# Kernel tuning notes

Hardware: AMD Instinct MI355X
Metric: run time of the kernel (lower is better)

The kernel has to match this reference:

```python
import jax, jax.numpy as jnp
import numpy as np
from math import sqrt

N_USERS = 60000
N_ITEMS = 40000
D = 64
B = 3
LAYERS = 2
E = 600000
BATCH = 2048
N_NODES = (N_USERS + 1) + (N_ITEMS + 1)
REG_WEIGHT = 1e-3
BPR_GAMMA = 1e-10


def setup_inputs() -> dict:
    key = jax.random.key(0)
    k0, k1, k2, k3, k4 = jax.random.split(key, 5)
    user_emb = jax.random.normal(k0, (N_USERS + 1, D), jnp.float32) * 0.1
    item_emb = jax.random.normal(k1, (N_ITEMS + 1, D), jnp.float32) * 0.1
    W = jnp.ones((B,), jnp.float32)
    edge_users = jax.random.randint(k2, (B, E), 1, N_USERS + 1)
    edge_items = jax.random.randint(k3, (B, E), 1, N_ITEMS + 1)
    batch_data = jax.random.randint(k4, (BATCH, B, 3), 1, N_ITEMS + 1)
    return dict(user_emb=user_emb, item_emb=item_emb, W=W,
                edge_users=edge_users, edge_items=edge_items,
                batch_data=batch_data)


def _lightgcn(emb, eu, ei, layers):
    # bipartite undirected graph: users <-> items (items offset by N_USERS+1)
    it = ei + (N_USERS + 1)
    src = jnp.concatenate([eu, it])
    dst = jnp.concatenate([it, eu])
    deg = jax.ops.segment_sum(jnp.ones_like(src, jnp.float32), src, N_NODES)
    norm = jax.lax.rsqrt(jnp.maximum(deg[src], 1.0)) * jax.lax.rsqrt(jnp.maximum(deg[dst], 1.0))
    out = emb
    cur = emb
    for _ in range(layers):
        cur = jax.ops.segment_sum(cur[src] * norm[:, None], dst, N_NODES)
        out = out + cur
    return out / (layers + 1)


def _mutual_attention(f):
    # f: [N, B, D]
    S = jnp.einsum('nid,njd->nij', f, f)          # [N, B, B] pairwise scores
    last = S[:, B - 1:B, :]                        # [N, 1, B]
    proj = S[:, :B - 1, :]                         # [N, B-1, B]
    # (last * proj) * last / (last^2 + eps)   (dim-1 is size 1, sums/norms trivial)
    clear = (last * proj) * last / (last * last + 1e-12)   # [N, B-1, B]
    scores = jnp.sum(clear, axis=1, keepdims=True) + last   # [N, 1, B]
    all_scores = jnp.concatenate([clear, scores], axis=1)   # [N, B, B]
    att = jax.nn.softmax(all_scores / sqrt(D), axis=-1)
    return jnp.einsum('nij,njd->nid', att, f)


def reference(user_emb, item_emb, W, edge_users, edge_items, batch_data):
    total0 = jnp.concatenate([user_emb, item_emb], axis=0)   # [N_NODES, D]
    # global graph = union of all behaviors
    g_eu = edge_users.reshape(-1)
    g_ei = edge_items.reshape(-1)
    all_emb = _lightgcn(total0, g_eu, g_ei, LAYERS)
    # per-behavior propagation
    u_list, i_list = [], []
    for b in range(B):
        eb = _lightgcn(all_emb, edge_users[b], edge_items[b], LAYERS)
        u_list.append(eb[:N_USERS + 1])
        i_list.append(eb[N_USERS + 1:])
    all_user = jnp.stack(u_list, axis=1)   # [n_users+1, B, D]
    all_item = jnp.stack(i_list, axis=1)   # [n_items+1, B, D]
    all_user = _mutual_attention(all_user)
    # item behaviour degree: interactions per item per behavior
    ones = jnp.ones((E,), jnp.float32)
    ibd = jnp.stack([jax.ops.segment_sum(ones, edge_items[b], N_ITEMS + 1)
                     for b in range(B)], axis=1)   # [n_items+1, B]
    weight = ibd * W
    weight = weight / (jnp.sum(weight, axis=1, keepdims=True) + 1e-8)
    item_final = jnp.sum(all_item * weight[:, :, None], axis=1)   # [n_items+1, D]
    total_loss = jnp.float32(0.0)
    for b in range(B):
        users = batch_data[:, b, 0]
        items = batch_data[:, b, 1:3]
        uf = all_user[:, b][users][:, None, :]      # [batch, 1, D]
        itf = item_final[items]                      # [batch, 2, D]
        scores = jnp.sum(uf * itf, axis=2)           # [batch, 2]
        total_loss = total_loss - jnp.mean(
            jnp.log(BPR_GAMMA + jax.nn.sigmoid(scores[:, 0] - scores[:, 1])))
    emb_loss = (jnp.linalg.norm(user_emb) + jnp.linalg.norm(item_emb)) / (N_ITEMS + 1)
    return total_loss + REG_WEIGHT * emb_loss
```

## Files before the change

### kernel.cpp

```cpp
#include <hip/hip_runtime.h>
#include <hip/hip_bf16.h>
#include <math.h>

#define NUQ 60001
#define NIQ 40001
#define NNQ 100002
#define DQ  64
#define EQ  600000
#define BQ  3
#define BATCHQ 2048
#define ROWW 32
#define NSLOT (BATCHQ * BQ)
#define NPAD 100004
#define ADJB 1200000
#define BLK_ELE 2048
#define NBLK ((NNQ + BLK_ELE - 1) / BLK_ELE)
#define RANGE 392
#define NRANGE 256
#define NBINS (BQ * NRANGE)
#define NBLKA 256
#define EPB ((BQ * EQ + NBLKA - 1) / NBLKA)

typedef float f32x2 __attribute__((ext_vector_type(2)));

__device__ __forceinline__ float wave_sum(float v) {
#pragma unroll
  for (int m = 32; m >= 1; m >>= 1) v += __shfl_xor(v, m, 64);
  return v;
}
__device__ __forceinline__ int wave_sum_i(int v) {
#pragma unroll
  for (int m = 32; m >= 1; m >>= 1) v += __shfl_xor(v, m, 64);
  return v;
}

__device__ __forceinline__ unsigned pack_bf2(float lo, float hi) {
  unsigned a = __float_as_uint(lo);
  unsigned b = __float_as_uint(hi);
  a = (a + 0x7FFFu + ((a >> 16) & 1u)) >> 16;
  b = (b + 0x7FFFu + ((b >> 16) & 1u)) >> 16;
  return a | (b << 16);
}
__device__ __forceinline__ float unpk_lo(unsigned u) { return __uint_as_float(u << 16); }
__device__ __forceinline__ float unpk_hi(unsigned u) { return __uint_as_float(u & 0xFFFF0000u); }

__device__ __forceinline__ void ntst_u32(unsigned* p, unsigned v) { __builtin_nontemporal_store(v, p); }
__device__ __forceinline__ void ntst_f32(float* p, float v) { __builtin_nontemporal_store(v, p); }
__device__ __forceinline__ float ntld_f32(const float* p) { return __builtin_nontemporal_load(p); }

__global__ void zero_i_k(int* __restrict__ p, int n) {
  int tid = blockIdx.x * blockDim.x + threadIdx.x;
  int stride = gridDim.x * blockDim.x;
  for (int i = tid; i < n; i += stride) p[i] = 0;
}

__global__ void sumsq_k(const float* __restrict__ p, int n, float* __restrict__ acc) {
  int tid = blockIdx.x * blockDim.x + threadIdx.x;
  int stride = gridDim.x * blockDim.x;
  float s = 0.f;
  for (int i = tid; i < n; i += stride) { float v = p[i]; s += v * v; }
  s = wave_sum(s);
  __shared__ float ws[4];
  if ((threadIdx.x & 63) == 0) ws[threadIdx.x >> 6] = s;
  __syncthreads();
  if (threadIdx.x == 0) atomicAdd(acc, ws[0] + ws[1] + ws[2] + ws[3]);
}

__global__ void binc_k(const int* __restrict__ eu, const int* __restrict__ ei,
                       unsigned* __restrict__ counts) {
  __shared__ unsigned h[NBINS];
  for (int i = threadIdx.x; i < NBINS; i += 256) h[i] = 0u;
  __syncthreads();
  int base = blockIdx.x * EPB;
  int end = base + EPB;
  if (end > BQ * EQ) end = BQ * EQ;
  for (int idx = base + threadIdx.x; idx < end; idx += 256) {
    int b = idx / EQ;
    int u = eu[idx];
    int it = ei[idx] + NUQ;
    atomicAdd(&h[b * NRANGE + u / RANGE], 1u);
    atomicAdd(&h[b * NRANGE + it / RANGE], 1u);
  }
  __syncthreads();
  for (int i = threadIdx.x; i < NBINS; i += 256)
    counts[(size_t)blockIdx.x * NBINS + i] = h[i];
}

__global__ void binscan1_k(const unsigned* __restrict__ counts,
                           unsigned* __restrict__ offs, unsigned* __restrict__ bintot) {
  int bin = blockIdx.x;
  int t = threadIdx.x;
  int lane = t & 63, wid = t >> 6;
  unsigned v = counts[(size_t)t * NBINS + bin];
  unsigned incl = v;
#pragma unroll
  for (int off = 1; off < 64; off <<= 1) {
    unsigned x = __shfl_up(incl, off, 64);
    if (lane >= off) incl += x;
  }
  __shared__ unsigned wsum[4];
  if (lane == 63) wsum[wid] = incl;
  __syncthreads();
  if (t == 0) {
    unsigned s = 0;
#pragma unroll
    for (int w = 0; w < 4; ++w) { unsigned x = wsum[w]; wsum[w] = s; s += x; }
  }
  __syncthreads();
  unsigned excl = incl - v + wsum[wid];
  offs[(size_t)t * NBINS + bin] = excl;
  if (t == 255) bintot[bin] = excl + v;
}

__global__ void binscan2_k(const unsigned* __restrict__ bintot,
                           unsigned* __restrict__ binstart) {
  int t = threadIdx.x;
  int lane = t & 63, wid = t >> 6;
  unsigned c0 = bintot[t * 3 + 0], c1 = bintot[t * 3 + 1], c2 = bintot[t * 3 + 2];
  unsigned tsum = c0 + c1 + c2;
  unsigned incl = tsum;
#pragma unroll
  for (int off = 1; off < 64; off <<= 1) {
    unsigned x = __shfl_up(incl, off, 64);
    if (lane >= off) incl += x;
  }
  __shared__ unsigned wsum[4];
  if (lane == 63) wsum[wid] = incl;
  __syncthreads();
  if (t == 0) {
    unsigned s = 0;
#pragma unroll
    for (int w = 0; w < 4; ++w) { unsigned x = wsum[w]; wsum[w] = s; s += x; }
  }
  __syncthreads();
  unsigned run = incl - tsum + wsum[wid];
  binstart[t * 3 + 0] = run; run += c0;
  binstart[t * 3 + 1] = run; run += c1;
  binstart[t * 3 + 2] = run; run += c2;
  if (t == 255) binstart[NBINS] = run;
}

__global__ void binfill_k(const int* __restrict__ eu, const int* __restrict__ ei,
                          const unsigned* __restrict__ offs,
                          const unsigned* __restrict__ binstart,
                          unsigned* __restrict__ records) {
  __shared__ unsigned cur[NBINS];
  for (int i = threadIdx.x; i < NBINS; i += 256)
    cur[i] = binstart[i] + offs[(size_t)blockIdx.x * NBINS + i];
  __syncthreads();
  int base = blockIdx.x * EPB;
  int end = base + EPB;
  if (end > BQ * EQ) end = BQ * EQ;
  for (int idx = base + threadIdx.x; idx < end; idx += 256) {
    int b = idx / EQ;
    int u = eu[idx];
    int itl = ei[idx];
    int it = itl + NUQ;
    unsigned p = atomicAdd(&cur[b * NRANGE + u / RANGE], 1u);
    records[p] = ((unsigned)(u % RANGE) << 16) | (unsigned)itl;
    unsigned q = atomicAdd(&cur[b * NRANGE + it / RANGE], 1u);
    records[q] = ((unsigned)(it % RANGE) << 16) | (unsigned)u;
  }
}

__global__ void bindeg_k(const unsigned* __restrict__ records,
                         const unsigned* __restrict__ binstart,
                         int* __restrict__ degB) {
  int bin = blockIdx.x;
  int b = bin / NRANGE;
  int r0 = (bin % NRANGE) * RANGE;
  __shared__ int h[RANGE];
  for (int i = threadIdx.x; i < RANGE; i += 256) h[i] = 0;
  __syncthreads();
  unsigned rs = binstart[bin], re = binstart[bin + 1];
  for (unsigned j = rs + threadIdx.x; j < re; j += 256)
    atomicAdd(&h[records[j] >> 16], 1);
  __syncthreads();
  int nval = NNQ - r0;
  if (nval > RANGE) nval = RANGE;
  int* deg = degB + (size_t)b * NPAD;
  for (int i = threadIdx.x; i < nval; i += 256) deg[r0 + i] = h[i];
}

__global__ void scan_p1_k(const int* __restrict__ degB, int* __restrict__ partial) {
  int b = blockIdx.x / NBLK;
  int blk = blockIdx.x % NBLK;
  const int* deg = degB + (size_t)b * NPAD;
  int base = blk * BLK_ELE + threadIdx.x * 8;
  int s = 0;
#pragma unroll
  for (int i = 0; i < 8; ++i) { int idx = base + i; if (idx < NNQ) s += deg[idx]; }
  s = wave_sum_i(s);
  __shared__ int lds[4];
  int wid = threadIdx.x >> 6;
  if ((threadIdx.x & 63) == 0) lds[wid] = s;
  __syncthreads();
  if (threadIdx.x == 0) partial[b * NBLK + blk] = lds[0] + lds[1] + lds[2] + lds[3];
}

__global__ void scan_p2_k(int* __restrict__ partial, int* __restrict__ rowptrB) {
  int wid = threadIdx.x >> 6;
  int lane = threadIdx.x & 63;
  if (wid >= BQ) return;
  int v = (lane < NBLK) ? partial[wid * NBLK + lane] : 0;
  int orig = v;
#pragma unroll
  for (int off = 1; off < 64; off <<= 1) {
    int t = __shfl_up(v, off, 64);
    if (lane >= off) v += t;
  }
  if (lane < NBLK) partial[wid * NBLK + lane] = v - orig;
  if (lane == NBLK - 1) rowptrB[(size_t)wid * NPAD + NNQ] = v;
}

__global__ void scan_p3_k(const int* __restrict__ degB, const int* __restrict__ partial,
                          int* __restrict__ rowptrB, float* __restrict__ invsqB) {
  int b = blockIdx.x / NBLK;
  int blk = blockIdx.x % NBLK;
  const int* deg = degB + (size_t)b * NPAD;
  int* rowptr = rowptrB + (size_t)b * NPAD;
  float* invsq = invsqB + (size_t)b * NPAD;
  int base = blk * BLK_ELE + threadIdx.x * 8;
  int d[8];
  int tsum = 0;
#pragma unroll
  for (int i = 0; i < 8; ++i) {
    int idx = base + i;
    d[i] = (idx < NNQ) ? deg[idx] : 0;
    tsum += d[i];
  }
  int lane = threadIdx.x & 63;
  int wid = threadIdx.x >> 6;
  int incl = tsum;
#pragma unroll
  for (int off = 1; off < 64; off <<= 1) {
    int t = __shfl_up(incl, off, 64);
    if (lane >= off) incl += t;
  }
  int excl = incl - tsum;
  __shared__ int lds[4];
  if (lane == 63) lds[wid] = incl;
  __syncthreads();
  if (threadIdx.x == 0) {
    int s = 0;
#pragma unroll
    for (int w = 0; w < 4; ++w) { int t = lds[w]; lds[w] = s; s += t; }
  }
  __syncthreads();
  int run = excl + lds[wid] + partial[b * NBLK + blk];
#pragma unroll
  for (int i = 0; i < 8; ++i) {
    int idx = base + i;
    if (idx < NNQ) {
      rowptr[idx] = run;
      run += d[i];
      invsq[idx] = rsqrtf(fmaxf((float)d[i], 1.f));
    }
  }
}

__global__ void invsqg_k(const int* __restrict__ degB, float* __restrict__ invsqG) {
  int n = blockIdx.x * blockDim.x + threadIdx.x;
  if (n >= NNQ) return;
  int dg = degB[n] + degB[NPAD + n] + degB[2 * NPAD + n];
  invsqG[n] = rsqrtf(fmaxf((float)dg, 1.f));
}

__global__ void binscat_k(const unsigned* __restrict__ records,
                          const unsigned* __restrict__ binstart,
                          const int* __restrict__ rowptrB,
                          unsigned short* __restrict__ adjB) {
  int bin = blockIdx.x;
  int b = bin / NRANGE;
  int r0 = (bin % NRANGE) * RANGE;
  int nval = NNQ - r0;
  if (nval > RANGE) nval = RANGE;
  __shared__ int cur[RANGE];
  const int* rowptr = rowptrB + (size_t)b * NPAD;
  for (int i = threadIdx.x; i < nval; i += 256) cur[i] = rowptr[r0 + i];
  __syncthreads();
  unsigned rs = binstart[bin], re = binstart[bin + 1];
  unsigned short* adj = adjB + (size_t)b * ADJB;
  for (unsigned j = rs + threadIdx.x; j < re; j += 256) {
    unsigned rec = records[j];
    int dl = rec >> 16;
    int pos = atomicAdd(&cur[dl], 1);
    adj[pos] = (unsigned short)(rec & 0xFFFFu);
  }
}

__global__ void pack_emb_k(const float* __restrict__ ue, const float* __restrict__ ie,
                           unsigned* __restrict__ E0) {
  int idx = blockIdx.x * blockDim.x + threadIdx.x;
  if (idx >= NNQ * ROWW) return;
  int n = idx >> 5, k = idx & 31;
  const float* src = (n < NUQ) ? (ue + (size_t)n * DQ) : (ie + (size_t)(n - NUQ) * DQ);
  float a = src[2 * k], b = src[2 * k + 1];
  ntst_u32(&E0[idx], pack_bf2(a, b));
}


__device__ __forceinline__ void gather_w32(const unsigned* __restrict__ S,
                                           const unsigned short* __restrict__ adj,
                                           const float* __restrict__ invsq,
                                           int start, int end, int offs,
                                           int l5, int g32, unsigned k4,
                                           float& alo, float& ahi) {
  for (int j0 = start; j0 < end; j0 += 32) {
    int nloc = end - j0;
    if (nloc > 32) nloc = 32;
    unsigned boff = (unsigned)offs << 7;
    float w = 0.f;
    if (l5 < nloc) {
      int a = (int)adj[j0 + l5] + offs;
      boff = (unsigned)a << 7;
      w = invsq[a];
    }
    for (int j = 0; j < nloc; j += 8) {
#pragma unroll
      for (int m = 0; m < 8; ++m) {
        int jj = j + m + g32;
        unsigned bo = (unsigned)__shfl((int)boff, jj, 64) + k4;
        float ww = __shfl(w, jj, 64);
        unsigned dd = *(const unsigned*)((const char*)S + bo);
        alo += ww * unpk_lo(dd);
        ahi += ww * unpk_hi(dd);
      }
    }
  }
}

__device__ __forceinline__ void gather3w32(const unsigned* __restrict__ S,
                                           const unsigned short* __restrict__ adjB,
                                           const float* __restrict__ wtab,
                                           int s0, int d0, int s1, int d1,
                                           int s2, int d2, int offs,
                                           int l5, int g32, unsigned k4,
                                           float& alo, float& ahi) {
  int D = d0 + d1 + d2;
  int d01 = d0 + d1;
  for (int j0 = 0; j0 < D; j0 += 32) {
    int nloc = D - j0;
    if (nloc > 32) nloc = 32;
    unsigned boff = (unsigned)offs << 7;
    float w = 0.f;
    int l = j0 + l5;
    if (l < D) {
      int idx;
      if (l < d0)       idx = s0 + l;
      else if (l < d01) idx = ADJB + s1 + (l - d0);
      else              idx = 2 * ADJB + s2 + (l - d01);
      int a = (int)adjB[idx] + offs;
      boff = (unsigned)a << 7;
      w = wtab[a];
    }
    for (int j = 0; j < nloc; j += 8) {
#pragma unroll
      for (int m = 0; m < 8; ++m) {
        int jj = j + m + g32;
        unsigned bo = (unsigned)__shfl((int)boff, jj, 64) + k4;
        float ww = __shfl(w, jj, 64);
        unsigned dd = *(const unsigned*)((const char*)S + bo);
        alo += ww * unpk_lo(dd);
        ahi += ww * unpk_hi(dd);
      }
    }
  }
}

__global__ void g_l1_k(const unsigned* __restrict__ E0, unsigned* __restrict__ T1,
                       const int* __restrict__ rowptrB, const unsigned short* __restrict__ adjB,
                       const float* __restrict__ invsqG) {
  int wv = (blockIdx.x * blockDim.x + threadIdx.x) >> 6;
  int lane = threadIdx.x & 63;
  int g = lane >> 5;
  int node = wv * 2 + g;
  if (node >= NNQ) return;
  int l5 = lane & 31, g32 = g << 5;
  unsigned k4 = (unsigned)l5 << 2;
  int offs = (node < NUQ) ? NUQ : 0;
  int s0 = rowptrB[node], d0 = rowptrB[node + 1] - s0;
  int s1 = rowptrB[NPAD + node], d1 = rowptrB[NPAD + node + 1] - s1;
  int s2 = rowptrB[2 * NPAD + node], d2 = rowptrB[2 * NPAD + node + 1] - s2;
  float alo = 0.f, ahi = 0.f;
  gather3w32(E0, adjB, invsqG, s0, d0, s1, d1, s2, d2, offs, l5, g32, k4, alo, ahi);
  float s = invsqG[node];
  ntst_u32(&T1[(size_t)node * ROWW + l5], pack_bf2(alo * s, ahi * s));
}

__global__ void g_l2c_k(const unsigned* __restrict__ E0, const unsigned* __restrict__ T1,
                        unsigned* __restrict__ C,
                        const int* __restrict__ rowptrB, const unsigned short* __restrict__ adjB,
                        const float* __restrict__ invsqG) {
  int wv = (blockIdx.x * blockDim.x + threadIdx.x) >> 6;
  int lane = threadIdx.x & 63;
  int g = lane >> 5;
  int node = wv * 2 + g;
  if (node >= NNQ) return;
  int l5 = lane & 31, g32 = g << 5;
  unsigned k4 = (unsigned)l5 << 2;
  int offs = (node < NUQ) ? NUQ : 0;
  int s0 = rowptrB[node], d0 = rowptrB[node + 1] - s0;
  int s1 = rowptrB[NPAD + node], d1 = rowptrB[NPAD + node + 1] - s1;
  int s2 = rowptrB[2 * NPAD + node], d2 = rowptrB[2 * NPAD + node + 1] - s2;
  float alo = 0.f, ahi = 0.f;
  gather3w32(T1, adjB, invsqG, s0, d0, s1, d1, s2, d2, offs, l5, g32, k4, alo, ahi);
  float s = invsqG[node];
  size_t rb = (size_t)node * ROWW + l5;
  unsigned e0 = E0[rb];
  unsigned t1 = T1[rb];
  float clo = (unpk_lo(e0) + unpk_lo(t1) + alo * s) * (1.f / 3.f);
  float chi = (unpk_hi(e0) + unpk_hi(t1) + ahi * s) * (1.f / 3.f);
  ntst_u32(&C[rb], pack_bf2(clo, chi));
}

__global__ void b_l1_k(const unsigned* __restrict__ C, unsigned* __restrict__ T1B,
                       const int* __restrict__ rowptrB, const unsigned short* __restrict__ adjB,
                       const float* __restrict__ invsqB) {
  int wv = (blockIdx.x * blockDim.x + threadIdx.x) >> 6;
  int lane = threadIdx.x & 63;
  int g = lane >> 5;
  int node = wv * 2 + g;
  if (node >= NNQ) return;
  int b = blockIdx.y;
  const int* rowptr = rowptrB + (size_t)b * NPAD;
  const float* iv = invsqB + (size_t)b * NPAD;
  int l5 = lane & 31, g32 = g << 5;
  unsigned k4 = (unsigned)l5 << 2;
  int offs = (node < NUQ) ? NUQ : 0;
  float alo = 0.f, ahi = 0.f;
  gather_w32(C, adjB + (size_t)b * ADJB, iv, rowptr[node], rowptr[node + 1], offs, l5, g32, k4, alo, ahi);
  float s = iv[node];
  ntst_u32(&T1B[(size_t)b * NNQ * ROWW + (size_t)node * ROWW + l5], pack_bf2(alo * s, ahi * s));
}

__global__ void slot_users_k(const unsigned* __restrict__ C, const unsigned* __restrict__ T1B,
                             const int* __restrict__ rowptrB, const unsigned short* __restrict__ adjB,
                             const float* __restrict__ invsqB,
                             const int* __restrict__ batch, float* __restrict__ UG) {
  int wv = (blockIdx.x * blockDim.x + threadIdx.x) >> 6;
  int lane = threadIdx.x & 63;
  int g = lane >> 5;
  int slot = wv * 2 + g;
  if (slot >= NSLOT) return;
  int b = blockIdx.y;
  const int* rp = rowptrB + (size_t)b * NPAD;
  const float* iv = invsqB + (size_t)b * NPAD;
  const unsigned* T1 = T1B + (size_t)b * NNQ * ROWW;
  int u = batch[slot * 3 + 0];
  int l5 = lane & 31, g32 = g << 5;
  unsigned k4 = (unsigned)l5 << 2;
  float alo = 0.f, ahi = 0.f;
  gather_w32(T1, adjB + (size_t)b * ADJB, iv, rp[u], rp[u + 1], NUQ, l5, g32, k4, alo, ahi);
  float s = iv[u];
  size_t rb = (size_t)u * ROWW + l5;
  unsigned c0 = C[rb];
  unsigned t0 = T1[rb];
  size_t base = ((size_t)slot * BQ + b) * DQ + 2 * l5;
  f32x2 o;
  o.x = (unpk_lo(c0) + unpk_lo(t0) + alo * s) * (1.f / 3.f);
  o.y = (unpk_hi(c0) + unpk_hi(t0) + ahi * s) * (1.f / 3.f);
  __builtin_nontemporal_store(o, (f32x2*)&UG[base]);
}

__global__ void slot_items_k(const unsigned* __restrict__ C, const unsigned* __restrict__ T1B,
                             const int* __restrict__ rowptrB, const unsigned short* __restrict__ adjB,
                             const float* __restrict__ invsqB,
                             const int* __restrict__ batch, float* __restrict__ IG) {
  int wv = (blockIdx.x * blockDim.x + threadIdx.x) >> 6;
  int lane = threadIdx.x & 63;
  int g = lane >> 5;
  int islot = wv * 2 + g;
  if (islot >= 2 * NSLOT) return;
  int b = blockIdx.y;
  const int* rp = rowptrB + (size_t)b * NPAD;
  const float* iv = invsqB + (size_t)b * NPAD;
  const unsigned* T1 = T1B + (size_t)b * NNQ * ROWW;
  int slot = islot >> 1;
  int c = (islot & 1) + 1;
  int n = batch[slot * 3 + c] + NUQ;
  int l5 = lane & 31, g32 = g << 5;
  unsigned k4 = (unsigned)l5 << 2;
  float alo = 0.f, ahi = 0.f;
  gather_w32(T1, adjB + (size_t)b * ADJB, iv, rp[n], rp[n + 1], 0, l5, g32, k4, alo, ahi);
  float s = iv[n];
  size_t rb = (size_t)n * ROWW + l5;
  unsigned c0 = C[rb];
  unsigned t0 = T1[rb];
  size_t base = ((size_t)islot * BQ + b) * DQ + 2 * l5;
  f32x2 o;
  o.x = (unpk_lo(c0) + unpk_lo(t0) + alo * s) * (1.f / 3.f);
  o.y = (unpk_hi(c0) + unpk_hi(t0) + ahi * s) * (1.f / 3.f);
  __builtin_nontemporal_store(o, (f32x2*)&IG[base]);
}

__global__ void epilogue_k(const float* __restrict__ UG, const float* __restrict__ IG,
                           const int* __restrict__ degB, const int* __restrict__ batch,
                           const float* __restrict__ W, float* __restrict__ acc) {
  int slot = (blockIdx.x * blockDim.x + threadIdx.x) >> 6;
  int lane = threadIdx.x & 63;
  float val = 0.f;
  if (slot < NSLOT) {
    int bb = slot % BQ;
    size_t base = (size_t)slot * (BQ * DQ) + lane;
    float a0 = ntld_f32(&UG[base]);
    float a1 = ntld_f32(&UG[base + 64]);
    float a2 = ntld_f32(&UG[base + 128]);
    float p00 = wave_sum(a0 * a0);
    float p01 = wave_sum(a0 * a1);
    float p02 = wave_sum(a0 * a2);
    float p11 = wave_sum(a1 * a1);
    float p12 = wave_sum(a1 * a2);
    float p22 = wave_sum(a2 * a2);
    float last[3] = {p02, p12, p22};
    float S0[3] = {p00, p01, p02};
    float S1[3] = {p01, p11, p12};
    float rows[3][3];
#pragma unroll
    for (int j = 0; j < 3; ++j) {
      float l = last[j];
      float f = l * l / (l * l + 1e-12f);
      float c0 = S0[j] * f;
      float c1 = S1[j] * f;
      rows[0][j] = c0;
      rows[1][j] = c1;
      rows[2][j] = c0 + c1 + l;
    }
    float x0 = rows[bb][0] * 0.125f, x1 = rows[bb][1] * 0.125f, x2 = rows[bb][2] * 0.125f;
    float m = fmaxf(x0, fmaxf(x1, x2));
    float e0 = expf(x0 - m), e1 = expf(x1 - m), e2 = expf(x2 - m);
    float inv = 1.f / (e0 + e1 + e2);
    float uf = (e0 * a0 + e1 * a1 + e2 * a2) * inv;
    float sco[2];
#pragma unroll
    for (int c = 0; c < 2; ++c) {
      int islot = slot * 2 + c;
      int node = batch[slot * 3 + 1 + c] + NUQ;
      float w0 = (float)degB[0 * NPAD + node] * W[0];
      float w1 = (float)degB[1 * NPAD + node] * W[1];
      float w2 = (float)degB[2 * NPAD + node] * W[2];
      float inv2 = 1.f / (w0 + w1 + w2 + 1e-8f);
      size_t rb = (size_t)islot * (BQ * DQ) + lane;
      float ifv = (ntld_f32(&IG[rb]) * w0 + ntld_f32(&IG[rb + 64]) * w1 +
                   ntld_f32(&IG[rb + 128]) * w2) * inv2;
      sco[c] = wave_sum(uf * ifv);
    }
    if (lane == 0) {
      float x = sco[0] - sco[1];
      float sg = 1.f / (1.f + expf(-x));
      val = -logf(1e-10f + sg) * (1.f / (float)BATCHQ);
    }
  }
  __shared__ float ws[4];
  if (lane == 0) ws[threadIdx.x >> 6] = val;
  __syncthreads();
  if (threadIdx.x == 0) atomicAdd(acc, ws[0] + ws[1] + ws[2] + ws[3]);
}

__global__ void finalize_k(const float* __restrict__ sc, unsigned int* __restrict__ out) {
  float total = sc[0] + 0.001f * (sqrtf(sc[1]) + sqrtf(sc[2])) / (float)NIQ;
  unsigned int bits = __float_as_uint(total);
  unsigned int lsb = (bits >> 16) & 1u;
  unsigned int rb = (bits + 0x7FFFu + lsb) >> 16;
  out[0] = (rb << 16) | rb;
}

extern "C" void kernel_launch(void* const* d_in, const int* in_sizes, int n_in,
                              void* d_out, int out_size, void* d_ws, size_t ws_size,
                              hipStream_t stream) {
  const float* ue = (const float*)d_in[0];
  const float* ie = (const float*)d_in[1];
  const float* W  = (const float*)d_in[2];
  const int* eu    = (const int*)d_in[3];
  const int* ei    = (const int*)d_in[4];
  const int* batch = (const int*)d_in[5];

  unsigned* E0  = (unsigned*)d_ws;
  unsigned* T1  = E0 + (size_t)NNQ * ROWW;
  unsigned* C   = T1 + (size_t)NNQ * ROWW;
  unsigned* T1B = C + (size_t)NNQ * ROWW;
  float* UG   = (float*)(T1B + (size_t)BQ * NNQ * ROWW);
  float* IG   = UG + (size_t)NSLOT * (BQ * DQ);
  unsigned short* adjB = (unsigned short*)(IG + (size_t)2 * NSLOT * (BQ * DQ));
  int* rowptrB= (int*)(adjB + (size_t)BQ * ADJB);
  int* degB   = rowptrB + 3 * NPAD;
  float* invsqB = (float*)(degB + 3 * NPAD);
  float* invsqG = invsqB + 3 * NPAD;
  unsigned* counts = (unsigned*)(invsqG + NPAD);
  unsigned* offs   = counts + (size_t)NBLKA * NBINS;
  unsigned* bintot = offs + (size_t)NBLKA * NBINS;
  unsigned* binstart = bintot + 1024;
  unsigned* records = binstart + 1024;
  int* partial  = (int*)(records + (size_t)2 * BQ * EQ);
  float* sc   = (float*)(partial + 256);

  zero_i_k<<<1, 64, 0, stream>>>((int*)sc, 8);
  sumsq_k<<<512, 256, 0, stream>>>(ue, NUQ * DQ, sc + 1);
  sumsq_k<<<512, 256, 0, stream>>>(ie, NIQ * DQ, sc + 2);

  binc_k<<<NBLKA, 256, 0, stream>>>(eu, ei, counts);
  binscan1_k<<<NBINS, 256, 0, stream>>>(counts, offs, bintot);
  binscan2_k<<<1, 256, 0, stream>>>(bintot, binstart);
  binfill_k<<<NBLKA, 256, 0, stream>>>(eu, ei, offs, binstart, records);
  bindeg_k<<<NBINS, 256, 0, stream>>>(records, binstart, degB);
  scan_p1_k<<<BQ * NBLK, 256, 0, stream>>>(degB, partial);
  scan_p2_k<<<1, 256, 0, stream>>>(partial, rowptrB);
  scan_p3_k<<<BQ * NBLK, 256, 0, stream>>>(degB, partial, rowptrB, invsqB);
  invsqg_k<<<(NNQ + 255) / 256, 256, 0, stream>>>(degB, invsqG);
  binscat_k<<<NBINS, 256, 0, stream>>>(records, binstart, rowptrB, adjB);

  pack_emb_k<<<(NNQ * ROWW + 255) / 256, 256, 0, stream>>>(ue, ie, E0);

  const int NODE_BLKS2 = (NNQ / 2 + 4) / 4;

  g_l1_k<<<NODE_BLKS2, 256, 0, stream>>>(E0, T1, rowptrB, adjB, invsqG);
  g_l2c_k<<<NODE_BLKS2, 256, 0, stream>>>(E0, T1, C, rowptrB, adjB, invsqG);

  b_l1_k<<<dim3(NODE_BLKS2, 3), 256, 0, stream>>>(C, T1B, rowptrB, adjB, invsqB);

  slot_users_k<<<dim3(NSLOT / 8, 3), 256, 0, stream>>>(C, T1B, rowptrB, adjB, invsqB, batch, UG);
  slot_items_k<<<dim3(2 * NSLOT / 8, 3), 256, 0, stream>>>(C, T1B, rowptrB, adjB, invsqB, batch, IG);
  epilogue_k<<<(NSLOT + 3) / 4, 256, 0, stream>>>(UG, IG, degB, batch, W, sc);
  finalize_k<<<1, 1, 0, stream>>>(sc, (unsigned int*)d_out);
}
```

Baseline: 415.8 us.

## Fuse slot gathers into epilogue and fold sum-of-squares into embedding pack

Merges the separate user-slot and item-slot gather kernels into the epilogue. Each wave now computes all three behaviours' layer-2 rows for its slot in registers, using a new 64-wide gather that splits neighbours between the two half-waves, so the UG/IG intermediate buffers are no longer written and re-read. It also computes the embedding L2 sums inside pack_emb_k, which removes two sumsq launches and a second pass over the input embeddings. The trade-off is less parallelism in the slot phase (one wave per slot doing nine gathers serially instead of separate grids per behaviour) plus extra atomics in the pack kernel.

```diff
diff --git a/kernel.cpp b/kernel.cpp
--- a/kernel.cpp
+++ b/kernel.cpp
@@ -45,25 +45,11 @@
 __device__ __forceinline__ float unpk_hi(unsigned u) { return __uint_as_float(u & 0xFFFF0000u); }
 
 __device__ __forceinline__ void ntst_u32(unsigned* p, unsigned v) { __builtin_nontemporal_store(v, p); }
-__device__ __forceinline__ void ntst_f32(float* p, float v) { __builtin_nontemporal_store(v, p); }
-__device__ __forceinline__ float ntld_f32(const float* p) { return __builtin_nontemporal_load(p); }
 
 __global__ void zero_i_k(int* __restrict__ p, int n) {
   int tid = blockIdx.x * blockDim.x + threadIdx.x;
   int stride = gridDim.x * blockDim.x;
   for (int i = tid; i < n; i += stride) p[i] = 0;
-}
-
-__global__ void sumsq_k(const float* __restrict__ p, int n, float* __restrict__ acc) {
-  int tid = blockIdx.x * blockDim.x + threadIdx.x;
-  int stride = gridDim.x * blockDim.x;
-  float s = 0.f;
-  for (int i = tid; i < n; i += stride) { float v = p[i]; s += v * v; }
-  s = wave_sum(s);
-  __shared__ float ws[4];
-  if ((threadIdx.x & 63) == 0) ws[threadIdx.x >> 6] = s;
-  __syncthreads();
-  if (threadIdx.x == 0) atomicAdd(acc, ws[0] + ws[1] + ws[2] + ws[3]);
 }
 
 __global__ void binc_k(const int* __restrict__ eu, const int* __restrict__ ei,
@@ -290,15 +276,30 @@
 }
 
 __global__ void pack_emb_k(const float* __restrict__ ue, const float* __restrict__ ie,
-                           unsigned* __restrict__ E0) {
+                           unsigned* __restrict__ E0, float* __restrict__ sc) {
   int idx = blockIdx.x * blockDim.x + threadIdx.x;
-  if (idx >= NNQ * ROWW) return;
-  int n = idx >> 5, k = idx & 31;
-  const float* src = (n < NUQ) ? (ue + (size_t)n * DQ) : (ie + (size_t)(n - NUQ) * DQ);
-  float a = src[2 * k], b = src[2 * k + 1];
-  ntst_u32(&E0[idx], pack_bf2(a, b));
-}
-
+  float su = 0.f, si = 0.f;
+  if (idx < NNQ * ROWW) {
+    int n = idx >> 5, k = idx & 31;
+    const float* src = (n < NUQ) ? (ue + (size_t)n * DQ) : (ie + (size_t)(n - NUQ) * DQ);
+    float a = src[2 * k], b = src[2 * k + 1];
+    ntst_u32(&E0[idx], pack_bf2(a, b));
+    float v = a * a + b * b;
+    if (n < NUQ) su = v; else si = v;
+  }
+  su = wave_sum(su);
+  si = wave_sum(si);
+  __shared__ float wsU[4], wsI[4];
+  int wid = threadIdx.x >> 6;
+  if ((threadIdx.x & 63) == 0) { wsU[wid] = su; wsI[wid] = si; }
+  __syncthreads();
+  if (threadIdx.x == 0) {
+    float tu = wsU[0] + wsU[1] + wsU[2] + wsU[3];
+    float ti = wsI[0] + wsI[1] + wsI[2] + wsI[3];
+    if (tu != 0.f) atomicAdd(sc + 1, tu);
+    if (ti != 0.f) atomicAdd(sc + 2, ti);
+  }
+}
 
 __device__ __forceinline__ void gather_w32(const unsigned* __restrict__ S,
                                            const unsigned short* __restrict__ adj,
@@ -358,6 +359,36 @@
 #pragma unroll
       for (int m = 0; m < 8; ++m) {
         int jj = j + m + g32;
+        unsigned bo = (unsigned)__shfl((int)boff, jj, 64) + k4;
+        float ww = __shfl(w, jj, 64);
+        unsigned dd = *(const unsigned*)((const char*)S + bo);
+        alo += ww * unpk_lo(dd);
+        ahi += ww * unpk_hi(dd);
+      }
+    }
+  }
+}
+
+__device__ __forceinline__ void gather_w64(const unsigned* __restrict__ S,
+                                           const unsigned short* __restrict__ adj,
+                                           const float* __restrict__ invsq,
+                                           int start, int end, int offs,
+                                           int lane, unsigned k4, int g,
+                                           float& alo, float& ahi) {
+  for (int j0 = start; j0 < end; j0 += 64) {
+    int nloc = end - j0;
+    if (nloc > 64) nloc = 64;
+    unsigned boff = (unsigned)offs << 7;
+    float w = 0.f;
+    if (lane < nloc) {
+      int a = (int)adj[j0 + lane] + offs;
+      boff = (unsigned)a << 7;
+      w = invsq[a];
+    }
+    for (int j = 0; j < nloc; j += 16) {
+#pragma unroll
+      for (int m = 0; m < 8; ++m) {
+        int jj = j + 2 * m + g;
         unsigned bo = (unsigned)__shfl((int)boff, jj, 64) + k4;
         float ww = __shfl(w, jj, 64);
         unsigned dd = *(const unsigned*)((const char*)S + bo);
@@ -434,84 +465,44 @@
   ntst_u32(&T1B[(size_t)b * NNQ * ROWW + (size_t)node * ROWW + l5], pack_bf2(alo * s, ahi * s));
 }
 
-__global__ void slot_users_k(const unsigned* __restrict__ C, const unsigned* __restrict__ T1B,
-                             const int* __restrict__ rowptrB, const unsigned short* __restrict__ adjB,
-                             const float* __restrict__ invsqB,
-                             const int* __restrict__ batch, float* __restrict__ UG) {
-  int wv = (blockIdx.x * blockDim.x + threadIdx.x) >> 6;
-  int lane = threadIdx.x & 63;
-  int g = lane >> 5;
-  int slot = wv * 2 + g;
-  if (slot >= NSLOT) return;
-  int b = blockIdx.y;
-  const int* rp = rowptrB + (size_t)b * NPAD;
-  const float* iv = invsqB + (size_t)b * NPAD;
-  const unsigned* T1 = T1B + (size_t)b * NNQ * ROWW;
-  int u = batch[slot * 3 + 0];
-  int l5 = lane & 31, g32 = g << 5;
-  unsigned k4 = (unsigned)l5 << 2;
-  float alo = 0.f, ahi = 0.f;
-  gather_w32(T1, adjB + (size_t)b * ADJB, iv, rp[u], rp[u + 1], NUQ, l5, g32, k4, alo, ahi);
-  float s = iv[u];
-  size_t rb = (size_t)u * ROWW + l5;
-  unsigned c0 = C[rb];
-  unsigned t0 = T1[rb];
-  size_t base = ((size_t)slot * BQ + b) * DQ + 2 * l5;
-  f32x2 o;
-  o.x = (unpk_lo(c0) + unpk_lo(t0) + alo * s) * (1.f / 3.f);
-  o.y = (unpk_hi(c0) + unpk_hi(t0) + ahi * s) * (1.f / 3.f);
-  __builtin_nontemporal_store(o, (f32x2*)&UG[base]);
-}
-
-__global__ void slot_items_k(const unsigned* __restrict__ C, const unsigned* __restrict__ T1B,
-                             const int* __restrict__ rowptrB, const unsigned short* __restrict__ adjB,
-                             const float* __restrict__ invsqB,
-                             const int* __restrict__ batch, float* __restrict__ IG) {
-  int wv = (blockIdx.x * blockDim.x + threadIdx.x) >> 6;
-  int lane = threadIdx.x & 63;
-  int g = lane >> 5;
-  int islot = wv * 2 + g;
-  if (islot >= 2 * NSLOT) return;
-  int b = blockIdx.y;
-  const int* rp = rowptrB + (size_t)b * NPAD;
-  const float* iv = invsqB + (size_t)b * NPAD;
-  const unsigned* T1 = T1B + (size_t)b * NNQ * ROWW;
-  int slot = islot >> 1;
-  int c = (islot & 1) + 1;
-  int n = batch[slot * 3 + c] + NUQ;
-  int l5 = lane & 31, g32 = g << 5;
-  unsigned k4 = (unsigned)l5 << 2;
-  float alo = 0.f, ahi = 0.f;
-  gather_w32(T1, adjB + (size_t)b * ADJB, iv, rp[n], rp[n + 1], 0, l5, g32, k4, alo, ahi);
-  float s = iv[n];
-  size_t rb = (size_t)n * ROWW + l5;
-  unsigned c0 = C[rb];
-  unsigned t0 = T1[rb];
-  size_t base = ((size_t)islot * BQ + b) * DQ + 2 * l5;
-  f32x2 o;
-  o.x = (unpk_lo(c0) + unpk_lo(t0) + alo * s) * (1.f / 3.f);
-  o.y = (unpk_hi(c0) + unpk_hi(t0) + ahi * s) * (1.f / 3.f);
-  __builtin_nontemporal_store(o, (f32x2*)&IG[base]);
-}
-
-__global__ void epilogue_k(const float* __restrict__ UG, const float* __restrict__ IG,
-                           const int* __restrict__ degB, const int* __restrict__ batch,
-                           const float* __restrict__ W, float* __restrict__ acc) {
+__global__ void mega_slot_k(const unsigned* __restrict__ C, const unsigned* __restrict__ T1B,
+                            const int* __restrict__ rowptrB, const unsigned short* __restrict__ adjB,
+                            const float* __restrict__ invsqB, const int* __restrict__ degB,
+                            const int* __restrict__ batch, const float* __restrict__ W,
+                            float* __restrict__ acc) {
   int slot = (blockIdx.x * blockDim.x + threadIdx.x) >> 6;
   int lane = threadIdx.x & 63;
   float val = 0.f;
   if (slot < NSLOT) {
+    int k = lane & 31, g = lane >> 5;
+    unsigned k4 = (unsigned)k << 2;
+    int u = batch[slot * 3 + 0];
+    f32x2 a0v, a1v, a2v;
+#pragma unroll
+    for (int b = 0; b < BQ; ++b) {
+      const int* rp = rowptrB + (size_t)b * NPAD;
+      const float* iv = invsqB + (size_t)b * NPAD;
+      const unsigned* T1 = T1B + (size_t)b * NNQ * ROWW;
+      float alo = 0.f, ahi = 0.f;
+      gather_w64(T1, adjB + (size_t)b * ADJB, iv, rp[u], rp[u + 1], NUQ, lane, k4, g, alo, ahi);
+      alo += __shfl_xor(alo, 32, 64);
+      ahi += __shfl_xor(ahi, 32, 64);
+      float s = iv[u];
+      size_t rb = (size_t)u * ROWW + k;
+      unsigned c0 = C[rb];
+      unsigned t0 = T1[rb];
+      f32x2 o;
+      o.x = (unpk_lo(c0) + unpk_lo(t0) + alo * s) * (1.f / 3.f);
+      o.y = (unpk_hi(c0) + unpk_hi(t0) + ahi * s) * (1.f / 3.f);
+      if (b == 0) a0v = o; else if (b == 1) a1v = o; else a2v = o;
+    }
+    float p00 = 0.5f * wave_sum(a0v.x * a0v.x + a0v.y * a0v.y);
+    float p01 = 0.5f * wave_sum(a0v.x * a1v.x + a0v.y * a1v.y);
+    float p02 = 0.5f * wave_sum(a0v.x * a2v.x + a0v.y * a2v.y);
+    float p11 = 0.5f * wave_sum(a1v.x * a1v.x + a1v.y * a1v.y);
+    float p12 = 0.5f * wave_sum(a1v.x * a2v.x + a1v.y * a2v.y);
+    float p22 = 0.5f * wave_sum(a2v.x * a2v.x + a2v.y * a2v.y);
     int bb = slot % BQ;
-    size_t base = (size_t)slot * (BQ * DQ) + lane;
-    float a0 = ntld_f32(&UG[base]);
-    float a1 = ntld_f32(&UG[base + 64]);
-    float a2 = ntld_f32(&UG[base + 128]);
-    float p00 = wave_sum(a0 * a0);
-    float p01 = wave_sum(a0 * a1);
-    float p02 = wave_sum(a0 * a2);
-    float p11 = wave_sum(a1 * a1);
-    float p12 = wave_sum(a1 * a2);
-    float p22 = wave_sum(a2 * a2);
     float last[3] = {p02, p12, p22};
     float S0[3] = {p00, p01, p02};
     float S1[3] = {p01, p11, p12};
@@ -530,20 +521,40 @@
     float m = fmaxf(x0, fmaxf(x1, x2));
     float e0 = expf(x0 - m), e1 = expf(x1 - m), e2 = expf(x2 - m);
     float inv = 1.f / (e0 + e1 + e2);
-    float uf = (e0 * a0 + e1 * a1 + e2 * a2) * inv;
+    f32x2 uf;
+    uf.x = (e0 * a0v.x + e1 * a1v.x + e2 * a2v.x) * inv;
+    uf.y = (e0 * a0v.y + e1 * a1v.y + e2 * a2v.y) * inv;
     float sco[2];
 #pragma unroll
     for (int c = 0; c < 2; ++c) {
-      int islot = slot * 2 + c;
       int node = batch[slot * 3 + 1 + c] + NUQ;
+      f32x2 i0v, i1v, i2v;
+#pragma unroll
+      for (int b = 0; b < BQ; ++b) {
+        const int* rp = rowptrB + (size_t)b * NPAD;
+        const float* iv = invsqB + (size_t)b * NPAD;
+        const unsigned* T1 = T1B + (size_t)b * NNQ * ROWW;
+        float alo = 0.f, ahi = 0.f;
+        gather_w64(T1, adjB + (size_t)b * ADJB, iv, rp[node], rp[node + 1], 0, lane, k4, g, alo, ahi);
+        alo += __shfl_xor(alo, 32, 64);
+        ahi += __shfl_xor(ahi, 32, 64);
+        float s = iv[node];
+        size_t rb = (size_t)node * ROWW + k;
+        unsigned c0 = C[rb];
+        unsigned t0 = T1[rb];
+        f32x2 o;
+        o.x = (unpk_lo(c0) + unpk_lo(t0) + alo * s) * (1.f / 3.f);
+        o.y = (unpk_hi(c0) + unpk_hi(t0) + ahi * s) * (1.f / 3.f);
+        if (b == 0) i0v = o; else if (b == 1) i1v = o; else i2v = o;
+      }
       float w0 = (float)degB[0 * NPAD + node] * W[0];
       float w1 = (float)degB[1 * NPAD + node] * W[1];
       float w2 = (float)degB[2 * NPAD + node] * W[2];
       float inv2 = 1.f / (w0 + w1 + w2 + 1e-8f);
-      size_t rb = (size_t)islot * (BQ * DQ) + lane;
-      float ifv = (ntld_f32(&IG[rb]) * w0 + ntld_f32(&IG[rb + 64]) * w1 +
-                   ntld_f32(&IG[rb + 128]) * w2) * inv2;
-      sco[c] = wave_sum(uf * ifv);
+      f32x2 ifv;
+      ifv.x = (i0v.x * w0 + i1v.x * w1 + i2v.x * w2) * inv2;
+      ifv.y = (i0v.y * w0 + i1v.y * w1 + i2v.y * w2) * inv2;
+      sco[c] = 0.5f * wave_sum(uf.x * ifv.x + uf.y * ifv.y);
     }
     if (lane == 0) {
       float x = sco[0] - sco[1];
@@ -579,9 +590,7 @@
   unsigned* T1  = E0 + (size_t)NNQ * ROWW;
   unsigned* C   = T1 + (size_t)NNQ * ROWW;
   unsigned* T1B = C + (size_t)NNQ * ROWW;
-  float* UG   = (float*)(T1B + (size_t)BQ * NNQ * ROWW);
-  float* IG   = UG + (size_t)NSLOT * (BQ * DQ);
-  unsigned short* adjB = (unsigned short*)(IG + (size_t)2 * NSLOT * (BQ * DQ));
+  unsigned short* adjB = (unsigned short*)(T1B + (size_t)BQ * NNQ * ROWW);
   int* rowptrB= (int*)(adjB + (size_t)BQ * ADJB);
   int* degB   = rowptrB + 3 * NPAD;
   float* invsqB = (float*)(degB + 3 * NPAD);
@@ -595,8 +604,6 @@
   float* sc   = (float*)(partial + 256);
 
   zero_i_k<<<1, 64, 0, stream>>>((int*)sc, 8);
-  sumsq_k<<<512, 256, 0, stream>>>(ue, NUQ * DQ, sc + 1);
-  sumsq_k<<<512, 256, 0, stream>>>(ie, NIQ * DQ, sc + 2);
 
   binc_k<<<NBLKA, 256, 0, stream>>>(eu, ei, counts);
   binscan1_k<<<NBINS, 256, 0, stream>>>(counts, offs, bintot);
@@ -609,7 +616,7 @@
   invsqg_k<<<(NNQ + 255) / 256, 256, 0, stream>>>(degB, invsqG);
   binscat_k<<<NBINS, 256, 0, stream>>>(records, binstart, rowptrB, adjB);
 
-  pack_emb_k<<<(NNQ * ROWW + 255) / 256, 256, 0, stream>>>(ue, ie, E0);
+  pack_emb_k<<<(NNQ * ROWW + 255) / 256, 256, 0, stream>>>(ue, ie, E0, sc);
 
   const int NODE_BLKS2 = (NNQ / 2 + 4) / 4;
 
@@ -618,8 +625,6 @@
 
   b_l1_k<<<dim3(NODE_BLKS2, 3), 256, 0, stream>>>(C, T1B, rowptrB, adjB, invsqB);
 
-  slot_users_k<<<dim3(NSLOT / 8, 3), 256, 0, stream>>>(C, T1B, rowptrB, adjB, invsqB, batch, UG);
-  slot_items_k<<<dim3(2 * NSLOT / 8, 3), 256, 0, stream>>>(C, T1B, rowptrB, adjB, invsqB, batch, IG);
-  epilogue_k<<<(NSLOT + 3) / 4, 256, 0, stream>>>(UG, IG, degB, batch, W, sc);
+  mega_slot_k<<<(NSLOT + 3) / 4, 256, 0, stream>>>(C, T1B, rowptrB, adjB, invsqB, degB, batch, W, sc);
   finalize_k<<<1, 1, 0, stream>>>(sc, (unsigned int*)d_out);
 }
```

Result: slower. 539.1 us (+29.7%).
